# Kernel optimization log

Measured on AMD Instinct MI355X. Metric: run time of the kernel, lower is better.

## Reference

```python
import jax, jax.numpy as jnp
import numpy as np


def setup_inputs() -> dict:
    key = jax.random.key(0)
    k1, k2, k3, k4 = jax.random.split(key, 4)
    B, C, T, H, W = 2, 64, 8, 48, 48
    C2 = C // 2
    x_in = jax.random.normal(k1, (B, C, T, H, W), dtype=jnp.float32)
    # per-time-slice 1x1 conv weights (theta/phi pairs), kaiming-ish scale
    theta_w = jax.random.normal(k2, (T, C2, C), dtype=jnp.float32) / np.sqrt(C)
    phi_w = jax.random.normal(k3, (T, C2, C), dtype=jnp.float32) / np.sqrt(C)
    out_w = jax.random.normal(k4, (C, C), dtype=jnp.float32) / np.sqrt(C)
    return {"x_in": x_in, "theta_w": theta_w, "phi_w": phi_w, "out_w": out_w}


def reference(x_in, theta_w, phi_w, out_w):
    B, C, T, H, W = x_in.shape
    C2 = theta_w.shape[1]
    P = H * W
    # [B, T, C, P] layout: flatten spatial, move time next to batch
    x = jnp.transpose(x_in, (0, 2, 1, 3, 4)).reshape(B, T, C, P)
    # per-slice 1x1 convs == per-slice channel matmuls with slice-specific weights
    theta = jnp.einsum("toc,btcp->btop", theta_w, x)  # [B,T,C2,P]
    phi = jnp.einsum("toc,btcp->btop", phi_w, x)      # [B,T,C2,P]
    scale = 1.0 / jnp.sqrt(jnp.asarray(C2, dtype=x_in.dtype))
    scores = jnp.einsum("btcp,btcq->btpq", theta, phi) * scale  # [B,T,P,P]
    attn = jax.nn.softmax(scores, axis=-1)
    f = jnp.einsum("btpq,btcq->btcp", attn, x)  # value = raw x, [B,T,C,P]
    # conv_out: 1x1x1 Conv3d (pointwise over channels), then residual
    out = jnp.einsum("oc,btcp->btop", out_w, f)
    out = jnp.transpose(out.reshape(B, T, C, H, W), (0, 2, 1, 3, 4))
    return out + x_in
```

## Files before the change

### kernel.cpp

```cpp
#include <hip/hip_runtime.h>
#include <hip/hip_bf16.h>

#define CC 64
#define TT 8
#define PP 2304
#define C2 32
#define BT 16
#define NKT 36
#define HKT 18
#define SCALE2 0.25503486f

using h8 = __attribute__((ext_vector_type(8))) _Float16;
using h4 = __attribute__((ext_vector_type(4))) _Float16;
using f4 = __attribute__((ext_vector_type(4))) float;

#if __has_builtin(__builtin_amdgcn_exp2f)
#define EXP2(v) __builtin_amdgcn_exp2f(v)
#else
#define EXP2(v) exp2f(v)
#endif

#define SWIZ_BT(xcd, g) ((xcd) + 8 * ((g) & 1))
#define SWIZ_PT(g) ((g) >> 1)


__global__ __launch_bounds__(256) void k_prep(
    const float* __restrict__ x, const float* __restrict__ tw,
    const float* __restrict__ pw, _Float16* __restrict__ thf,
    _Float16* __restrict__ rec) {
  const int qt = SWIZ_PT(blockIdx.y), bt = SWIZ_BT(blockIdx.x, blockIdx.y);
  const int b = bt >> 3, t = bt & 7;
  const int tid = threadIdx.x;
  const int wv = tid >> 6, lane = tid & 63;
  const int quad = lane >> 4, l15 = lane & 15;

  __shared__ __align__(16) float x_s[64][68];
  __shared__ __align__(16) _Float16 th_s[4][16][32];
  __shared__ __align__(16) _Float16 ph_s[4][16][32];

  const size_t xslice = ((size_t)b * CC * TT + t) * PP;
  const int qg0 = qt * 64;

  {
    const int qq = tid & 63;
    const int c0 = (tid >> 6) * 16;
#pragma unroll
    for (int i = 0; i < 16; i++) {
      int c = c0 + i;
      x_s[qq][c] = x[xslice + (size_t)c * (TT * PP) + qg0 + qq];
    }
  }
  __syncthreads();

  h8 bx[2];
#pragma unroll
  for (int ks = 0; ks < 2; ks++) {
    const float* row = &x_s[wv * 16 + l15][ks * 32 + quad * 8];
    float4 u0 = *reinterpret_cast<const float4*>(row);
    float4 u1 = *reinterpret_cast<const float4*>(row + 4);
    bx[ks][0] = (_Float16)u0.x; bx[ks][1] = (_Float16)u0.y;
    bx[ks][2] = (_Float16)u0.z; bx[ks][3] = (_Float16)u0.w;
    bx[ks][4] = (_Float16)u1.x; bx[ks][5] = (_Float16)u1.y;
    bx[ks][6] = (_Float16)u1.z; bx[ks][7] = (_Float16)u1.w;
  }

  const float* twt = tw + t * C2 * CC;
  const float* pwt = pw + t * C2 * CC;
  const f4 zero = {0.f, 0.f, 0.f, 0.f};
  f4 accT[2] = {zero, zero}, accP[2] = {zero, zero};
#pragma unroll
  for (int mt = 0; mt < 2; mt++)
#pragma unroll
    for (int ks = 0; ks < 2; ks++) {
      const float* wr = twt + (mt * 16 + l15) * CC + ks * 32 + quad * 8;
      const float* pr = pwt + (mt * 16 + l15) * CC + ks * 32 + quad * 8;
      float4 a0 = *reinterpret_cast<const float4*>(wr);
      float4 a1 = *reinterpret_cast<const float4*>(wr + 4);
      float4 p0 = *reinterpret_cast<const float4*>(pr);
      float4 p1 = *reinterpret_cast<const float4*>(pr + 4);
      h8 at = {(_Float16)a0.x, (_Float16)a0.y, (_Float16)a0.z, (_Float16)a0.w,
               (_Float16)a1.x, (_Float16)a1.y, (_Float16)a1.z, (_Float16)a1.w};
      h8 ap = {(_Float16)p0.x, (_Float16)p0.y, (_Float16)p0.z, (_Float16)p0.w,
               (_Float16)p1.x, (_Float16)p1.y, (_Float16)p1.z, (_Float16)p1.w};
      accT[mt] =
          __builtin_amdgcn_mfma_f32_16x16x32_f16(at, bx[ks], accT[mt], 0, 0, 0);
      accP[mt] =
          __builtin_amdgcn_mfma_f32_16x16x32_f16(ap, bx[ks], accP[mt], 0, 0, 0);
    }

#pragma unroll
  for (int mt = 0; mt < 2; mt++) {
    h4 tv, pv;
#pragma unroll
    for (int r = 0; r < 4; r++) {
      tv[r] = (_Float16)(accT[mt][r] * SCALE2);
      pv[r] = (_Float16)accP[mt][r];
    }
    *reinterpret_cast<h4*>(&th_s[wv][l15][mt * 16 + quad * 4]) = tv;
    *reinterpret_cast<h4*>(&ph_s[wv][l15][mt * 16 + quad * 4]) = pv;
  }

  h8 tfrag = *reinterpret_cast<const h8*>(&th_s[wv][l15][quad * 8]);
  *reinterpret_cast<h8*>(
      thf + (((size_t)(bt * NKT + qt) * 4 + wv) * 64 + lane) * 8) = tfrag;

  _Float16* rb = rec + (size_t)(bt * NKT + qt) * 6144;
  h8 pfrag = *reinterpret_cast<const h8*>(&ph_s[wv][l15][quad * 8]);
  *reinterpret_cast<h8*>(rb + wv * 512 + lane * 8) = pfrag;

#pragma unroll
  for (int ctp = 0; ctp < 2; ctp++) {
    h8 v;
#pragma unroll
    for (int j = 0; j < 4; j++) {
      v[j] = (_Float16)x_s[wv * 16 + quad * 4 + j][(2 * ctp) * 16 + l15];
      v[4 + j] = (_Float16)x_s[wv * 16 + quad * 4 + j][(2 * ctp + 1) * 16 + l15];
    }
    *reinterpret_cast<h8*>(rb + 2048 + (wv * 2 + ctp) * 512 + lane * 8) = v;
  }
}

__global__ __launch_bounds__(256, 3) void k_attn(
    const float* __restrict__ x, const _Float16* __restrict__ thf,
    const _Float16* __restrict__ rec, const float* __restrict__ ow,
    float* __restrict__ out) {
  const int pt = SWIZ_PT(blockIdx.y), bt = SWIZ_BT(blockIdx.x, blockIdx.y);
  const int b = bt >> 3, t = bt & 7;
  const int tid = threadIdx.x;
  const int wv = tid >> 6, lane = tid & 63;
  const int quad = lane >> 4, l15 = lane & 15;
  const int qg = wv & 1, kg = wv >> 1;

  __shared__ __align__(16) char smem[49152];
  _Float16* stage = reinterpret_cast<_Float16*>(smem);
  float* exch = reinterpret_cast<float*>(smem);
  float* out_s = reinterpret_cast<float*>(smem + 20480);

  h8 b_th[2];
#pragma unroll
  for (int ps = 0; ps < 2; ps++)
    b_th[ps] = *reinterpret_cast<const h8*>(
        thf + (((size_t)(bt * NKT + pt) * 4 + qg * 2 + ps) * 64 + lane) * 8);

  const _Float16* recb = rec + (size_t)bt * NKT * 6144;

  int ch_tile[6], ch_off[6];
#pragma unroll
  for (int j = 0; j < 6; j++) {
    int m = wv * 6 + j;
    ch_tile[j] = m / 12;
    ch_off[j] = (m % 12) * 512 + lane * 8;
  }

  int4 v[6];
#pragma unroll
  for (int j = 0; j < 6; j++) {
    v[j] = *reinterpret_cast<const int4*>(
        recb + (size_t)(ch_tile[j] * HKT) * 6144 + ch_off[j]);
    *reinterpret_cast<int4*>(stage + ch_tile[j] * 6144 + ch_off[j]) = v[j];
  }

  const f4 zero = {0.f, 0.f, 0.f, 0.f};
  f4 O[2][4] = {{zero, zero, zero, zero}, {zero, zero, zero, zero}};
  float l_sum[2] = {0.f, 0.f};

  for (int i = 0; i < HKT; i++) {
    __syncthreads();
    const _Float16* cur = stage + (i & 1) * 12288 + kg * 6144;

    if (i < HKT - 1) {
#pragma unroll
      for (int j = 0; j < 6; j++)
        v[j] = *reinterpret_cast<const int4*>(
            recb + (size_t)(ch_tile[j] * HKT + i + 1) * 6144 + ch_off[j]);
    }

    h8 aphi[4];
#pragma unroll
    for (int nt = 0; nt < 4; nt++)
      aphi[nt] = *reinterpret_cast<const h8*>(cur + nt * 512 + lane * 8);
    f4 s[4][2];
#pragma unroll
    for (int nt = 0; nt < 4; nt++)
#pragma unroll
      for (int ps = 0; ps < 2; ps++)
        s[nt][ps] = __builtin_amdgcn_mfma_f32_16x16x32_f16(aphi[nt], b_th[ps],
                                                           zero, 0, 0, 0);

#pragma unroll
    for (int nt = 0; nt < 4; nt++) {
      h4 bw[2];
#pragma unroll
      for (int ps = 0; ps < 2; ps++)
#pragma unroll
        for (int r = 0; r < 4; r++) {
          float w = EXP2(s[nt][ps][r]);
          l_sum[ps] += w;
          bw[ps][r] = (_Float16)w;
        }
#pragma unroll
      for (int ctp = 0; ctp < 2; ctp++) {
        h8 xx = *reinterpret_cast<const h8*>(cur + 2048 + (nt * 2 + ctp) * 512 +
                                             lane * 8);
        h4 a0 = __builtin_shufflevector(xx, xx, 0, 1, 2, 3);
        h4 a1 = __builtin_shufflevector(xx, xx, 4, 5, 6, 7);
#pragma unroll
        for (int ps = 0; ps < 2; ps++) {
          O[ps][2 * ctp] = __builtin_amdgcn_mfma_f32_16x16x16f16(
              a0, bw[ps], O[ps][2 * ctp], 0, 0, 0);
          O[ps][2 * ctp + 1] = __builtin_amdgcn_mfma_f32_16x16x16f16(
              a1, bw[ps], O[ps][2 * ctp + 1], 0, 0, 0);
        }
      }
    }

    if (i < HKT - 1) {
#pragma unroll
      for (int j = 0; j < 6; j++)
        *reinterpret_cast<int4*>(stage + ((i + 1) & 1) * 12288 +
                                 ch_tile[j] * 6144 + ch_off[j]) = v[j];
    }
  }

#pragma unroll
  for (int ps = 0; ps < 2; ps++) {
    l_sum[ps] += __shfl_xor(l_sum[ps], 16);
    l_sum[ps] += __shfl_xor(l_sum[ps], 32);
  }

  __syncthreads();

  if (kg == 1) {
#pragma unroll
    for (int ps = 0; ps < 2; ps++) {
#pragma unroll
      for (int k = 0; k < 16; k++)
        exch[((qg * 2 + ps) * 17 + k) * 64 + lane] = O[ps][k >> 2][k & 3];
      exch[((qg * 2 + ps) * 17 + 16) * 64 + lane] = l_sum[ps];
    }
  }
  __syncthreads();

  if (kg == 0) {
#pragma unroll
    for (int ps = 0; ps < 2; ps++) {
#pragma unroll
      for (int k = 0; k < 16; k++)
        O[ps][k >> 2][k & 3] += exch[((qg * 2 + ps) * 17 + k) * 64 + lane];
      const float inv =
          1.f / (l_sum[ps] + exch[((qg * 2 + ps) * 17 + 16) * 64 + lane]);

      h4 bf[4];
#pragma unroll
      for (int ct = 0; ct < 4; ct++)
#pragma unroll
        for (int r = 0; r < 4; r++) bf[ct][r] = (_Float16)(O[ps][ct][r] * inv);

      f4 D3[4] = {zero, zero, zero, zero};
#pragma unroll
      for (int mt = 0; mt < 4; mt++)
#pragma unroll
        for (int ct = 0; ct < 4; ct++) {
          const float* wrow =
              ow + (size_t)(mt * 16 + l15) * CC + ct * 16 + quad * 4;
          float4 u = *reinterpret_cast<const float4*>(wrow);
          h4 aw = {(_Float16)u.x, (_Float16)u.y, (_Float16)u.z, (_Float16)u.w};
          D3[mt] =
              __builtin_amdgcn_mfma_f32_16x16x16f16(aw, bf[ct], D3[mt], 0, 0, 0);
        }

#pragma unroll
      for (int mt = 0; mt < 4; mt++)
#pragma unroll
        for (int r = 0; r < 4; r++)
          out_s[(mt * 16 + quad * 4 + r) * 68 + (qg * 2 + ps) * 16 + l15] =
              D3[mt][r];
    }
  }
  __syncthreads();

  const int co = tid >> 2;
  const int psub = (tid & 3) * 16;
  const size_t gbase = ((size_t)(b * CC + co) * TT + t) * PP + pt * 64 + psub;
#pragma unroll
  for (int jj = 0; jj < 4; jj++) {
    float4 vo =
        *reinterpret_cast<const float4*>(&out_s[co * 68 + psub + jj * 4]);
    float4 xr = *reinterpret_cast<const float4*>(&x[gbase + jj * 4]);
    vo.x += xr.x; vo.y += xr.y; vo.z += xr.z; vo.w += xr.w;
    *reinterpret_cast<float4*>(&out[gbase + jj * 4]) = vo;
  }
}

extern "C" void kernel_launch(void* const* d_in, const int* in_sizes, int n_in,
                              void* d_out, int out_size, void* d_ws,
                              size_t ws_size, hipStream_t stream) {
  (void)in_sizes; (void)n_in; (void)out_size; (void)ws_size;
  const float* x = (const float*)d_in[0];
  const float* tw = (const float*)d_in[1];
  const float* pw = (const float*)d_in[2];
  const float* ow = (const float*)d_in[3];
  float* out = (float*)d_out;

  _Float16* thf = (_Float16*)d_ws;
  _Float16* rec = thf + (size_t)BT * NKT * 4 * 64 * 8;

  k_prep<<<dim3(8, 72), 256, 0, stream>>>(x, tw, pw, thf, rec);
  k_attn<<<dim3(8, 72), 256, 0, stream>>>(x, thf, rec, ow, out);
}
```

Measured before the change: 113.5 us.

## Load key tiles directly into registers instead of staging through LDS

Each wave now loads its own phi/x key tile fragments from global memory straight into registers, double-buffered in register arrays (cur/nxt). This replaces the cooperative LDS staging with per-iteration __syncthreads. Dropping the shared-memory round trip and the barriers is meant to cut synchronisation and LDS traffic. In exchange, each wave issues redundant global loads for data that two query-group waves share, and register pressure rises (24 int4 buffers), which could lower occupancy under launch_bounds(256,3).

```diff
diff --git a/kernel.cpp b/kernel.cpp
--- a/kernel.cpp
+++ b/kernel.cpp
@@ -131,10 +131,8 @@
   const int quad = lane >> 4, l15 = lane & 15;
   const int qg = wv & 1, kg = wv >> 1;
 
-  __shared__ __align__(16) char smem[49152];
-  _Float16* stage = reinterpret_cast<_Float16*>(smem);
-  float* exch = reinterpret_cast<float*>(smem);
-  float* out_s = reinterpret_cast<float*>(smem + 20480);
+  __shared__ __align__(16) float exch[4 * 17 * 64];
+  __shared__ __align__(16) float out_s[64 * 68];
 
   h8 b_th[2];
 #pragma unroll
@@ -142,50 +140,35 @@
     b_th[ps] = *reinterpret_cast<const h8*>(
         thf + (((size_t)(bt * NKT + pt) * 4 + qg * 2 + ps) * 64 + lane) * 8);
 
-  const _Float16* recb = rec + (size_t)bt * NKT * 6144;
-
-  int ch_tile[6], ch_off[6];
-#pragma unroll
-  for (int j = 0; j < 6; j++) {
-    int m = wv * 6 + j;
-    ch_tile[j] = m / 12;
-    ch_off[j] = (m % 12) * 512 + lane * 8;
-  }
-
-  int4 v[6];
-#pragma unroll
-  for (int j = 0; j < 6; j++) {
-    v[j] = *reinterpret_cast<const int4*>(
-        recb + (size_t)(ch_tile[j] * HKT) * 6144 + ch_off[j]);
-    *reinterpret_cast<int4*>(stage + ch_tile[j] * 6144 + ch_off[j]) = v[j];
-  }
+  const _Float16* mybase =
+      rec + ((size_t)bt * NKT + (size_t)kg * HKT) * 6144 + lane * 8;
+
+  int4 cur[12], nxt[12];
+#pragma unroll
+  for (int j = 0; j < 12; j++)
+    cur[j] = *reinterpret_cast<const int4*>(mybase + j * 512);
 
   const f4 zero = {0.f, 0.f, 0.f, 0.f};
   f4 O[2][4] = {{zero, zero, zero, zero}, {zero, zero, zero, zero}};
   float l_sum[2] = {0.f, 0.f};
 
   for (int i = 0; i < HKT; i++) {
-    __syncthreads();
-    const _Float16* cur = stage + (i & 1) * 12288 + kg * 6144;
-
     if (i < HKT - 1) {
-#pragma unroll
-      for (int j = 0; j < 6; j++)
-        v[j] = *reinterpret_cast<const int4*>(
-            recb + (size_t)(ch_tile[j] * HKT + i + 1) * 6144 + ch_off[j]);
-    }
-
-    h8 aphi[4];
-#pragma unroll
-    for (int nt = 0; nt < 4; nt++)
-      aphi[nt] = *reinterpret_cast<const h8*>(cur + nt * 512 + lane * 8);
+      const _Float16* nb = mybase + (size_t)(i + 1) * 6144;
+#pragma unroll
+      for (int j = 0; j < 12; j++)
+        nxt[j] = *reinterpret_cast<const int4*>(nb + j * 512);
+    }
+
     f4 s[4][2];
 #pragma unroll
-    for (int nt = 0; nt < 4; nt++)
+    for (int nt = 0; nt < 4; nt++) {
+      h8 aphi = *reinterpret_cast<const h8*>(&cur[nt]);
 #pragma unroll
       for (int ps = 0; ps < 2; ps++)
-        s[nt][ps] = __builtin_amdgcn_mfma_f32_16x16x32_f16(aphi[nt], b_th[ps],
+        s[nt][ps] = __builtin_amdgcn_mfma_f32_16x16x32_f16(aphi, b_th[ps],
                                                            zero, 0, 0, 0);
+    }
 
 #pragma unroll
     for (int nt = 0; nt < 4; nt++) {
@@ -200,8 +183,7 @@
         }
 #pragma unroll
       for (int ctp = 0; ctp < 2; ctp++) {
-        h8 xx = *reinterpret_cast<const h8*>(cur + 2048 + (nt * 2 + ctp) * 512 +
-                                             lane * 8);
+        h8 xx = *reinterpret_cast<const h8*>(&cur[4 + nt * 2 + ctp]);
         h4 a0 = __builtin_shufflevector(xx, xx, 0, 1, 2, 3);
         h4 a1 = __builtin_shufflevector(xx, xx, 4, 5, 6, 7);
 #pragma unroll
@@ -216,9 +198,7 @@
 
     if (i < HKT - 1) {
 #pragma unroll
-      for (int j = 0; j < 6; j++)
-        *reinterpret_cast<int4*>(stage + ((i + 1) & 1) * 12288 +
-                                 ch_tile[j] * 6144 + ch_off[j]) = v[j];
+      for (int j = 0; j < 12; j++) cur[j] = nxt[j];
     }
   }
 
@@ -227,8 +207,6 @@
     l_sum[ps] += __shfl_xor(l_sum[ps], 16);
     l_sum[ps] += __shfl_xor(l_sum[ps], 32);
   }
-
-  __syncthreads();
 
   if (kg == 1) {
 #pragma unroll
```

New measurement: 110.3 us. -2.8%, faster.
